# Kernel optimization log

Measured on AMD Instinct MI355X. Metric: run time of the kernel, lower is better.

Reference implementation:

```python
import jax, jax.numpy as jnp
import numpy as np

EPS = 1e-12  # F.normalize default eps

def _l2norm(x, axis):
    n = jnp.maximum(jnp.linalg.norm(x, axis=axis, keepdims=True), EPS)
    return x / n

def setup_inputs() -> dict:
    key = jax.random.key(0)
    k1, k2 = jax.random.split(key)
    B, G, D, K = 256, 100, 768, 128
    h = jax.random.normal(k1, (B, G, D), dtype=jnp.float32)
    duplicate_pooling = jax.random.normal(k2, (G, D, K), dtype=jnp.float32)
    out_extrap = jnp.zeros((B, G, K), dtype=jnp.float32)
    return {"h": h, "duplicate_pooling": duplicate_pooling, "out_extrap": out_extrap}

def reference(h, duplicate_pooling, out_extrap):
    # normalize=True: L2-normalize each h[:, i, :] over feature dim (dim=1 of the
    # flattened [B, D] view == last axis), and each w_i = W[i] over dim=0 (the D axis).
    hn = _l2norm(h, axis=-1)                       # [B, G, D]
    wn = _l2norm(duplicate_pooling, axis=1)        # [G, D, K]
    # Fused grouped batched GEMM over all G groups at once.
    out = jnp.einsum('bgd,gdk->bgk', hn, wn)       # [B, G, K]
    return out
```

## Files before the change

kernel.cpp:

```cpp
#include <hip/hip_runtime.h>

#define Gn   100
#define Bn   256
#define Dn   768
#define Kn   128
#define LDP  40

typedef __attribute__((ext_vector_type(8))) short short8;
typedef __attribute__((ext_vector_type(4))) float f32x4;

__device__ inline unsigned pack2(float lo, float hi) {
  union { float f; unsigned u; } a, b; a.f = lo; b.f = hi;
  return __builtin_amdgcn_perm(b.u + 0x8000u, a.u + 0x8000u, 0x07060302u);
}

__device__ inline void barrier_nodrain() {
  asm volatile("s_waitcnt lgkmcnt(0)\n\ts_barrier" ::: "memory");
}

__global__ __launch_bounds__(256) void groupfc_kernel(
    const float* __restrict__ h, const float* __restrict__ W,
    float* __restrict__ out) {
  const int id   = blockIdx.x;
  const int xcd  = id & 7;
  const int rest = id >> 3;
  const int tl   = rest & 7;
  const int g    = (rest >> 3) * 8 + xcd;
  if (g >= Gn) return;
  const int mt   = tl >> 1;
  const int nt   = tl & 1;

  const int t    = threadIdx.x;
  const int lane = t & 63;
  const int wave = t >> 6;
  const int wm   = wave >> 1, wn = wave & 1;
  const int l15  = lane & 15, quad = lane >> 4;

  __shared__ __align__(16) short Af[3][64 * LDP];
  __shared__ __align__(16) short Bf[3][64 * LDP];
  __shared__ float AssqL[64];
  __shared__ float BssqL[4][64];

  f32x4 acc00 = {0.f,0.f,0.f,0.f};
  f32x4 acc01 = acc00, acc10 = acc00, acc11 = acc00;

  const int ar = t >> 2;
  const int ac = (t & 3) * 8;
  const float* aptr = h + ((size_t)(mt * 64 + ar) * Gn + g) * Dn + ac;
  const int bk = t & 63;
  const int bq = t >> 6;
  const float* bptr = W + (size_t)g * (Dn * Kn) + (size_t)(bq * 8) * Kn + nt * 64 + bk;

  const int koff = quad * 8;
  const int m0   = wm * 32 + l15;
  const int n0   = wn * 32 + l15;

  float assq = 0.f, bssq = 0.f;
  float4 Ar[2][2];
  float  Br[2][8];

  auto load_set = [&](int c, int s) {
    const int d0 = c * 32;
    Ar[s][0] = *(const float4*)(aptr + d0);
    Ar[s][1] = *(const float4*)(aptr + d0 + 4);
#pragma unroll
    for (int i = 0; i < 8; ++i) Br[s][i] = bptr[(size_t)(d0 + i) * Kn];
  };

  auto pack_set = [&](int c, int s) {
    const float4 a0 = Ar[s][0], a1 = Ar[s][1];
    assq += a0.x*a0.x + a0.y*a0.y + a0.z*a0.z + a0.w*a0.w
          + a1.x*a1.x + a1.y*a1.y + a1.z*a1.z + a1.w*a1.w;
    uint4 ap;
    ap.x = pack2(a0.x, a0.y); ap.y = pack2(a0.z, a0.w);
    ap.z = pack2(a1.x, a1.y); ap.w = pack2(a1.z, a1.w);
    *(uint4*)&Af[c % 3][ar * LDP + ac] = ap;

    uint4 bp;
    bp.x = pack2(Br[s][0], Br[s][1]); bp.y = pack2(Br[s][2], Br[s][3]);
    bp.z = pack2(Br[s][4], Br[s][5]); bp.w = pack2(Br[s][6], Br[s][7]);
#pragma unroll
    for (int i = 0; i < 8; ++i) bssq += Br[s][i] * Br[s][i];
    *(uint4*)&Bf[c % 3][bk * LDP + bq * 8] = bp;
  };

  load_set(0, 0);
  load_set(1, 1);
  pack_set(0, 0);

#pragma unroll
  for (int c = 0; c < 24; ++c) {
    if (c + 2 < 24) load_set(c + 2, c & 1);
    if (c + 1 < 24) pack_set(c + 1, (c + 1) & 1);
    barrier_nodrain();

    const int b = c % 3;
    short8 af0 = *(const short8*)&Af[b][m0 * LDP + koff];
    short8 af1 = *(const short8*)&Af[b][(m0 + 16) * LDP + koff];
    short8 bf0 = *(const short8*)&Bf[b][n0 * LDP + koff];
    short8 bf1 = *(const short8*)&Bf[b][(n0 + 16) * LDP + koff];

    acc00 = __builtin_amdgcn_mfma_f32_16x16x32_bf16(af0, bf0, acc00, 0, 0, 0);
    acc01 = __builtin_amdgcn_mfma_f32_16x16x32_bf16(af0, bf1, acc01, 0, 0, 0);
    acc10 = __builtin_amdgcn_mfma_f32_16x16x32_bf16(af1, bf0, acc10, 0, 0, 0);
    acc11 = __builtin_amdgcn_mfma_f32_16x16x32_bf16(af1, bf1, acc11, 0, 0, 0);
  }

  assq += __shfl_xor(assq, 1);
  assq += __shfl_xor(assq, 2);
  if ((t & 3) == 0) AssqL[ar] = assq;
  BssqL[bq][bk] = bssq;
  __syncthreads();

  const float ws0 = BssqL[0][n0] + BssqL[1][n0] + BssqL[2][n0] + BssqL[3][n0];
  const float ws1 = BssqL[0][n0+16] + BssqL[1][n0+16] + BssqL[2][n0+16] + BssqL[3][n0+16];
  const float wi0 = 1.0f / fmaxf(sqrtf(ws0), 1e-12f);
  const float wi1 = 1.0f / fmaxf(sqrtf(ws1), 1e-12f);

#pragma unroll
  for (int mi = 0; mi < 2; ++mi) {
#pragma unroll
    for (int r = 0; r < 4; ++r) {
      const int lr = wm * 32 + mi * 16 + quad * 4 + r;
      const float hs = 1.0f / fmaxf(sqrtf(AssqL[lr]), 1e-12f);
      const float v0 = (mi ? acc10[r] : acc00[r]) * hs * wi0;
      const float v1 = (mi ? acc11[r] : acc01[r]) * hs * wi1;
      const int row = mt * 64 + lr;
      const size_t ob = ((size_t)row * Gn + g) * Kn + nt * 64;
      out[ob + wn * 32 + l15]      = v0;
      out[ob + wn * 32 + l15 + 16] = v1;
    }
  }
}

extern "C" void kernel_launch(void* const* d_in, const int* in_sizes, int n_in,
                              void* d_out, int out_size, void* d_ws, size_t ws_size,
                              hipStream_t stream) {
  const float* h = (const float*)d_in[0];
  const float* W = (const float*)d_in[1];
  float* out = (float*)d_out;
  hipLaunchKernelGGL(groupfc_kernel, dim3(832), dim3(256), 0, stream, h, W, out);
}
```

Baseline: 169.5 us.

## Enlarge block tile to 128x128 with 4x4 MFMA per wave

Each block now computes a 128x128 output tile per group instead of 64x64, so each wave issues a 4x4 grid of 16x16x32 bf16 MFMAs per K step. This halves how often h and W are re-read from global memory, and the grid shrinks from 832 to 208 blocks. LDS padding also changes from 40 to 36 shorts. The costs are fewer blocks than CUs, heavier register pressure from 64 accumulator floats plus the load staging, and LDS rows that are no longer 16-byte aligned for the vector stores and reads.

Result: slower. 255.6 us (+50.8%).

```diff
diff --git a/kernel.cpp b/kernel.cpp
--- a/kernel.cpp
+++ b/kernel.cpp
@@ -4,7 +4,7 @@
 #define Bn   256
 #define Dn   768
 #define Kn   128
-#define LDP  40
+#define LDP  36
 
 typedef __attribute__((ext_vector_type(8))) short short8;
 typedef __attribute__((ext_vector_type(4))) float f32x4;
@@ -21,14 +21,12 @@
 __global__ __launch_bounds__(256) void groupfc_kernel(
     const float* __restrict__ h, const float* __restrict__ W,
     float* __restrict__ out) {
-  const int id   = blockIdx.x;
-  const int xcd  = id & 7;
-  const int rest = id >> 3;
-  const int tl   = rest & 7;
-  const int g    = (rest >> 3) * 8 + xcd;
+  const int id  = blockIdx.x;
+  const int xcd = id & 7;
+  const int q   = id >> 3;
+  const int g   = (q >> 1) * 8 + xcd;
   if (g >= Gn) return;
-  const int mt   = tl >> 1;
-  const int nt   = tl & 1;
+  const int mt  = q & 1;
 
   const int t    = threadIdx.x;
   const int lane = t & 63;
@@ -36,99 +34,108 @@
   const int wm   = wave >> 1, wn = wave & 1;
   const int l15  = lane & 15, quad = lane >> 4;
 
-  __shared__ __align__(16) short Af[3][64 * LDP];
-  __shared__ __align__(16) short Bf[3][64 * LDP];
-  __shared__ float AssqL[64];
-  __shared__ float BssqL[4][64];
+  __shared__ __align__(16) short Af[3][128 * LDP];
+  __shared__ __align__(16) short Bf[3][128 * LDP];
+  __shared__ float AssqL[128];
+  __shared__ float BssqL[2][128];
 
-  f32x4 acc00 = {0.f,0.f,0.f,0.f};
-  f32x4 acc01 = acc00, acc10 = acc00, acc11 = acc00;
+  f32x4 acc[4][4];
+#pragma unroll
+  for (int i = 0; i < 4; ++i)
+#pragma unroll
+    for (int j = 0; j < 4; ++j) acc[i][j] = f32x4{0.f, 0.f, 0.f, 0.f};
 
-  const int ar = t >> 2;
-  const int ac = (t & 3) * 8;
-  const float* aptr = h + ((size_t)(mt * 64 + ar) * Gn + g) * Dn + ac;
-  const int bk = t & 63;
-  const int bq = t >> 6;
-  const float* bptr = W + (size_t)g * (Dn * Kn) + (size_t)(bq * 8) * Kn + nt * 64 + bk;
+  const int ar = t >> 1;
+  const int ac = (t & 1) * 16;
+  const float* aptr = h + ((size_t)(mt * 128 + ar) * Gn + g) * Dn + ac;
+  const int bn = t & 127;
+  const int bq = t >> 7;
+  const float* bptr = W + (size_t)g * (Dn * Kn) + (size_t)(bq * 16) * Kn + bn;
 
   const int koff = quad * 8;
-  const int m0   = wm * 32 + l15;
-  const int n0   = wn * 32 + l15;
 
   float assq = 0.f, bssq = 0.f;
-  float4 Ar[2][2];
-  float  Br[2][8];
+  float4 Ar[2][4];
+  float  Br[2][16];
 
   auto load_set = [&](int c, int s) {
     const int d0 = c * 32;
-    Ar[s][0] = *(const float4*)(aptr + d0);
-    Ar[s][1] = *(const float4*)(aptr + d0 + 4);
 #pragma unroll
-    for (int i = 0; i < 8; ++i) Br[s][i] = bptr[(size_t)(d0 + i) * Kn];
+    for (int i = 0; i < 4; ++i) Ar[s][i] = *(const float4*)(aptr + d0 + i * 4);
+#pragma unroll
+    for (int i = 0; i < 16; ++i) Br[s][i] = bptr[(size_t)(d0 + i) * Kn];
   };
 
   auto pack_set = [&](int c, int s) {
-    const float4 a0 = Ar[s][0], a1 = Ar[s][1];
-    assq += a0.x*a0.x + a0.y*a0.y + a0.z*a0.z + a0.w*a0.w
-          + a1.x*a1.x + a1.y*a1.y + a1.z*a1.z + a1.w*a1.w;
-    uint4 ap;
-    ap.x = pack2(a0.x, a0.y); ap.y = pack2(a0.z, a0.w);
-    ap.z = pack2(a1.x, a1.y); ap.w = pack2(a1.z, a1.w);
-    *(uint4*)&Af[c % 3][ar * LDP + ac] = ap;
+    const int b = c % 3;
+    uint4 ap0, ap1;
+    ap0.x = pack2(Ar[s][0].x, Ar[s][0].y); ap0.y = pack2(Ar[s][0].z, Ar[s][0].w);
+    ap0.z = pack2(Ar[s][1].x, Ar[s][1].y); ap0.w = pack2(Ar[s][1].z, Ar[s][1].w);
+    ap1.x = pack2(Ar[s][2].x, Ar[s][2].y); ap1.y = pack2(Ar[s][2].z, Ar[s][2].w);
+    ap1.z = pack2(Ar[s][3].x, Ar[s][3].y); ap1.w = pack2(Ar[s][3].z, Ar[s][3].w);
+#pragma unroll
+    for (int i = 0; i < 4; ++i) {
+      const float4 v = Ar[s][i];
+      assq += v.x*v.x + v.y*v.y + v.z*v.z + v.w*v.w;
+    }
+    *(uint4*)&Af[b][ar * LDP + ac]     = ap0;
+    *(uint4*)&Af[b][ar * LDP + ac + 8] = ap1;
 
-    uint4 bp;
-    bp.x = pack2(Br[s][0], Br[s][1]); bp.y = pack2(Br[s][2], Br[s][3]);
-    bp.z = pack2(Br[s][4], Br[s][5]); bp.w = pack2(Br[s][6], Br[s][7]);
+    uint4 bp0, bp1;
+    bp0.x = pack2(Br[s][0],  Br[s][1]);  bp0.y = pack2(Br[s][2],  Br[s][3]);
+    bp0.z = pack2(Br[s][4],  Br[s][5]);  bp0.w = pack2(Br[s][6],  Br[s][7]);
+    bp1.x = pack2(Br[s][8],  Br[s][9]);  bp1.y = pack2(Br[s][10], Br[s][11]);
+    bp1.z = pack2(Br[s][12], Br[s][13]); bp1.w = pack2(Br[s][14], Br[s][15]);
 #pragma unroll
-    for (int i = 0; i < 8; ++i) bssq += Br[s][i] * Br[s][i];
-    *(uint4*)&Bf[c % 3][bk * LDP + bq * 8] = bp;
+    for (int i = 0; i < 16; ++i) bssq += Br[s][i] * Br[s][i];
+    *(uint4*)&Bf[b][bn * LDP + bq * 16]     = bp0;
+    *(uint4*)&Bf[b][bn * LDP + bq * 16 + 8] = bp1;
   };
 
   load_set(0, 0);
   load_set(1, 1);
   pack_set(0, 0);
 
-#pragma unroll
   for (int c = 0; c < 24; ++c) {
     if (c + 2 < 24) load_set(c + 2, c & 1);
     if (c + 1 < 24) pack_set(c + 1, (c + 1) & 1);
     barrier_nodrain();
 
     const int b = c % 3;
-    short8 af0 = *(const short8*)&Af[b][m0 * LDP + koff];
-    short8 af1 = *(const short8*)&Af[b][(m0 + 16) * LDP + koff];
-    short8 bf0 = *(const short8*)&Bf[b][n0 * LDP + koff];
-    short8 bf1 = *(const short8*)&Bf[b][(n0 + 16) * LDP + koff];
-
-    acc00 = __builtin_amdgcn_mfma_f32_16x16x32_bf16(af0, bf0, acc00, 0, 0, 0);
-    acc01 = __builtin_amdgcn_mfma_f32_16x16x32_bf16(af0, bf1, acc01, 0, 0, 0);
-    acc10 = __builtin_amdgcn_mfma_f32_16x16x32_bf16(af1, bf0, acc10, 0, 0, 0);
-    acc11 = __builtin_amdgcn_mfma_f32_16x16x32_bf16(af1, bf1, acc11, 0, 0, 0);
+    short8 af[4], bf[4];
+#pragma unroll
+    for (int i = 0; i < 4; ++i) {
+      af[i] = *(const short8*)&Af[b][(wm * 64 + i * 16 + l15) * LDP + koff];
+      bf[i] = *(const short8*)&Bf[b][(wn * 64 + i * 16 + l15) * LDP + koff];
+    }
+#pragma unroll
+    for (int i = 0; i < 4; ++i)
+#pragma unroll
+      for (int j = 0; j < 4; ++j)
+        acc[i][j] = __builtin_amdgcn_mfma_f32_16x16x32_bf16(af[i], bf[j], acc[i][j], 0, 0, 0);
   }
 
   assq += __shfl_xor(assq, 1);
-  assq += __shfl_xor(assq, 2);
-  if ((t & 3) == 0) AssqL[ar] = assq;
-  BssqL[bq][bk] = bssq;
+  if ((t & 1) == 0) AssqL[ar] = assq;
+  BssqL[bq][bn] = bssq;
   __syncthreads();
 
-  const float ws0 = BssqL[0][n0] + BssqL[1][n0] + BssqL[2][n0] + BssqL[3][n0];
-  const float ws1 = BssqL[0][n0+16] + BssqL[1][n0+16] + BssqL[2][n0+16] + BssqL[3][n0+16];
-  const float wi0 = 1.0f / fmaxf(sqrtf(ws0), 1e-12f);
-  const float wi1 = 1.0f / fmaxf(sqrtf(ws1), 1e-12f);
-
+  float wi[4];
 #pragma unroll
-  for (int mi = 0; mi < 2; ++mi) {
+  for (int j = 0; j < 4; ++j) {
+    const int n = wn * 64 + j * 16 + l15;
+    wi[j] = 1.0f / fmaxf(sqrtf(BssqL[0][n] + BssqL[1][n]), 1e-12f);
+  }
+#pragma unroll
+  for (int i = 0; i < 4; ++i) {
 #pragma unroll
     for (int r = 0; r < 4; ++r) {
-      const int lr = wm * 32 + mi * 16 + quad * 4 + r;
+      const int lr = wm * 64 + i * 16 + quad * 4 + r;
       const float hs = 1.0f / fmaxf(sqrtf(AssqL[lr]), 1e-12f);
-      const float v0 = (mi ? acc10[r] : acc00[r]) * hs * wi0;
-      const float v1 = (mi ? acc11[r] : acc01[r]) * hs * wi1;
-      const int row = mt * 64 + lr;
-      const size_t ob = ((size_t)row * Gn + g) * Kn + nt * 64;
-      out[ob + wn * 32 + l15]      = v0;
-      out[ob + wn * 32 + l15 + 16] = v1;
+      const size_t ob = ((size_t)(mt * 128 + lr) * Gn + g) * Kn;
+#pragma unroll
+      for (int j = 0; j < 4; ++j)
+        out[ob + wn * 64 + j * 16 + l15] = acc[i][j][r] * hs * wi[j];
     }
   }
 }
@@ -139,5 +146,5 @@
   const float* h = (const float*)d_in[0];
   const float* W = (const float*)d_in[1];
   float* out = (float*)d_out;
-  hipLaunchKernelGGL(groupfc_kernel, dim3(832), dim3(256), 0, stream, h, W, out);
+  hipLaunchKernelGGL(groupfc_kernel, dim3(208), dim3(256), 0, stream, h, W, out);
 }
```
